# Performance work log

Measured on AMD Instinct MI355X. Metric: run time of the kernel, lower is better.

The kernel has to match this reference:

```python
import jax, jax.numpy as jnp
import numpy as np

NUM_USERS = 100000
NUM_ITEMS = 50000
EMB = 64
N_EDGES = 4800000
N_NODES = NUM_USERS + NUM_ITEMS
NEG_SLOPE = 0.01  # torch F.leaky_relu default


def setup_inputs() -> dict:
    key = jax.random.key(0)
    ks = jax.random.split(key, 12)
    inp = {
        "user_indices": jnp.arange(NUM_USERS, dtype=jnp.int32),
        "item_indices": jnp.arange(NUM_ITEMS, dtype=jnp.int32),
        "adj_rows": jax.random.randint(ks[0], (N_EDGES,), 0, N_NODES, dtype=jnp.int32),
        "adj_cols": jax.random.randint(ks[1], (N_EDGES,), 0, N_NODES, dtype=jnp.int32),
        "adj_vals": jax.random.uniform(ks[2], (N_EDGES,), dtype=jnp.float32),
        "user_emb": jax.random.normal(ks[3], (NUM_USERS, EMB), dtype=jnp.float32),
        "item_emb": jax.random.normal(ks[4], (NUM_ITEMS, EMB), dtype=jnp.float32),
    }
    # two propagation layers (layers=[64,64,64] -> zip gives 2 Linear pairs)
    s = 1.0 / np.sqrt(EMB)
    for li, kb in zip(range(2), range(5, 12, 4)):
        inp[f"W_gc{li}"] = jax.random.uniform(ks[kb], (EMB, EMB), jnp.float32, -s, s)
        inp[f"b_gc{li}"] = jax.random.uniform(ks[kb + 1], (EMB,), jnp.float32, -s, s)
        inp[f"W_bi{li}"] = jax.random.uniform(ks[kb + 2], (EMB, EMB), jnp.float32, -s, s)
        inp[f"b_bi{li}"] = jax.random.uniform(ks[kb + 3], (EMB,), jnp.float32, -s, s)
    return inp


def reference(user_indices, item_indices, adj_rows, adj_cols, adj_vals,
              user_emb, item_emb,
              W_gc0, b_gc0, W_bi0, b_bi0,
              W_gc1, b_gc1, W_bi1, b_bi1):
    ego = jnp.concatenate([user_emb[user_indices], item_emb[item_indices]], axis=0)  # [N, 64]
    n_nodes = ego.shape[0]
    all_embeddings = [ego]
    layer_params = [(W_gc0, b_gc0, W_bi0, b_bi0), (W_gc1, b_gc1, W_bi1, b_bi1)]
    for Wg, bg, Wb, bb in layer_params:
        # sparse adj @ ego : gather by col, scale by val, scatter-add by row
        side = jax.ops.segment_sum(adj_vals[:, None] * ego[adj_cols], adj_rows,
                                   num_segments=n_nodes)  # [N, 64]
        sum_emb = jax.nn.leaky_relu(side @ Wg.T + bg, NEG_SLOPE)
        bi_emb = jax.nn.leaky_relu((ego * side) @ Wb.T + bb, NEG_SLOPE)
        ego = sum_emb + bi_emb
        all_embeddings.append(ego)
    all_embeddings = jnp.concatenate(all_embeddings, axis=1)  # [N, 192]
    n_users = user_indices.shape[0]
    return all_embeddings[:n_users], all_embeddings[n_users:]
```

## Files before the change

### kernel.cpp

```cpp
#include <hip/hip_runtime.h>

#define NUSERS 100000
#define NITEMS 50000
#define NNODES 150000
#define EMB 64
#define NEDGES 4800000
#define OUTC 192
#define NEG_SLOPE 0.01f

#define BKT_SHIFT 10
#define NB 147
#define G 1024
#define EPB 4688
#define NSCAN (NB * G)
#define NSLICE 10
#define SLICE_SHIFT 14
#define NBINS (1024 * NSLICE)

typedef __attribute__((ext_vector_type(8))) short bf16x8;
typedef __attribute__((ext_vector_type(4))) float f32x4;

__device__ __forceinline__ unsigned short f2bf(float f) {
    unsigned u = __float_as_uint(f);
    unsigned r = (u + 0x7fffu + ((u >> 16) & 1u)) >> 16;
    return (unsigned short)r;
}
__device__ __forceinline__ float bf2f(short s) {
    return __uint_as_float(((unsigned)(unsigned short)s) << 16);
}

__global__ void build_ego(const int* __restrict__ ui, const int* __restrict__ ii,
                          const float* __restrict__ uemb, const float* __restrict__ iemb,
                          float* __restrict__ out, unsigned short* __restrict__ egoc) {
    int gid = blockIdx.x * blockDim.x + threadIdx.x;
    int r = gid >> 4, p = gid & 15;
    if (r >= NNODES) return;
    const float* src = (r < NUSERS) ? (uemb + (size_t)ui[r] * EMB)
                                    : (iemb + (size_t)ii[r - NUSERS] * EMB);
    float4 v = ((const float4*)src)[p];
    *(float4*)(out + (size_t)r * OUTC + p * 4) = v;
    ushort4 o;
    o.x = f2bf(v.x); o.y = f2bf(v.y); o.z = f2bf(v.z); o.w = f2bf(v.w);
    *(ushort4*)(egoc + (size_t)r * EMB + p * 4) = o;
}

__global__ void conv_w4(const float* __restrict__ s0, const float* __restrict__ s1,
                        const float* __restrict__ s2, const float* __restrict__ s3,
                        unsigned short* __restrict__ d0, unsigned short* __restrict__ d1,
                        unsigned short* __restrict__ d2, unsigned short* __restrict__ d3) {
    int i = blockIdx.x * 256 + threadIdx.x;
    if (i < 4096) {
        d0[i] = f2bf(s0[i]); d1[i] = f2bf(s1[i]);
        d2[i] = f2bf(s2[i]); d3[i] = f2bf(s3[i]);
    }
}

__global__ __launch_bounds__(256) void bucket_hist(const int* __restrict__ rows,
                                                   int* __restrict__ hist) {
    __shared__ int h[NB];
    int tid = threadIdx.x, blk = blockIdx.x;
    if (tid < NB) h[tid] = 0;
    __syncthreads();
    int q0 = blk * (EPB / 4), q1 = q0 + (EPB / 4);
    const int qmax = NEDGES / 4;
    if (q1 > qmax) q1 = qmax;
    for (int q = q0 + tid; q < q1; q += 256) {
        int4 r4 = ((const int4*)rows)[q];
        atomicAdd(&h[r4.x >> BKT_SHIFT], 1);
        atomicAdd(&h[r4.y >> BKT_SHIFT], 1);
        atomicAdd(&h[r4.z >> BKT_SHIFT], 1);
        atomicAdd(&h[r4.w >> BKT_SHIFT], 1);
    }
    __syncthreads();
    if (tid < NB) hist[(size_t)tid * G + blk] = h[tid];
}

__global__ void scan_chunk(const int* __restrict__ counts, int* __restrict__ outp,
                           int* __restrict__ blksum, int n) {
    __shared__ int buf[1024];
    int tid = threadIdx.x;
    int gid = blockIdx.x * 1024 + tid;
    int v = (gid < n) ? counts[gid] : 0;
    buf[tid] = v;
    __syncthreads();
    for (int off = 1; off < 1024; off <<= 1) {
        int t = (tid >= off) ? buf[tid - off] : 0;
        __syncthreads();
        buf[tid] += t;
        __syncthreads();
    }
    if (gid < n) outp[gid + 1] = buf[tid];
    if (tid == 1023) blksum[blockIdx.x] = buf[tid];
}

__global__ void scan_sums(int* __restrict__ blksum, int n) {
    __shared__ int buf[256];
    int tid = threadIdx.x;
    int v = (tid < n) ? blksum[tid] : 0;
    buf[tid] = v;
    __syncthreads();
    for (int off = 1; off < 256; off <<= 1) {
        int t = (tid >= off) ? buf[tid - off] : 0;
        __syncthreads();
        buf[tid] += t;
        __syncthreads();
    }
    if (tid < n) blksum[tid] = buf[tid] - v;
}

__global__ void add_offsets(int* __restrict__ outp, const int* __restrict__ blksum, int n) {
    int gid = blockIdx.x * 1024 + threadIdx.x;
    if (gid < n) outp[gid + 1] += blksum[blockIdx.x];
    if (gid == 0) outp[0] = 0;
}

__global__ __launch_bounds__(256) void bucket_scatter(
        const int* __restrict__ rows, const int* __restrict__ cols,
        const float* __restrict__ vals, const int* __restrict__ base,
        int2* __restrict__ bedge) {
    __shared__ int cur[NB];
    int tid = threadIdx.x, blk = blockIdx.x;
    if (tid < NB) cur[tid] = base[(size_t)tid * G + blk];
    __syncthreads();
    int q0 = blk * (EPB / 4), q1 = q0 + (EPB / 4);
    const int qmax = NEDGES / 4;
    if (q1 > qmax) q1 = qmax;
    for (int q = q0 + tid; q < q1; q += 256) {
        int4   r4 = ((const int4*)rows)[q];
        int4   c4 = ((const int4*)cols)[q];
        float4 v4 = ((const float4*)vals)[q];
        int s0 = atomicAdd(&cur[r4.x >> BKT_SHIFT], 1);
        bedge[s0] = make_int2(c4.x | ((r4.x & 1023) << 18), __float_as_int(v4.x));
        int s1 = atomicAdd(&cur[r4.y >> BKT_SHIFT], 1);
        bedge[s1] = make_int2(c4.y | ((r4.y & 1023) << 18), __float_as_int(v4.y));
        int s2 = atomicAdd(&cur[r4.z >> BKT_SHIFT], 1);
        bedge[s2] = make_int2(c4.z | ((r4.z & 1023) << 18), __float_as_int(v4.z));
        int s3 = atomicAdd(&cur[r4.w >> BKT_SHIFT], 1);
        bedge[s3] = make_int2(c4.w | ((r4.w & 1023) << 18), __float_as_int(v4.w));
    }
}

__global__ __launch_bounds__(1024) void bucket_csr(
        const int2* __restrict__ bedge, const int* __restrict__ base,
        int* __restrict__ rowptr, int2* __restrict__ csr) {
    __shared__ int h[NBINS];
    __shared__ int tsum[1024];
    int tid = threadIdx.x, bkt = blockIdx.x;
    int s  = base[(size_t)bkt * G];
    int e2 = base[(size_t)(bkt + 1) * G];
    for (int i = tid; i < NBINS; i += 1024) h[i] = 0;
    __syncthreads();
    for (int i = s + tid; i < e2; i += 1024) {
        int x = bedge[i].x;
        int bin = (x >> 18) * NSLICE + (((unsigned)x & 0x3FFFFu) >> SLICE_SHIFT);
        atomicAdd(&h[bin], 1);
    }
    __syncthreads();
    int b0 = tid * NSLICE;
    int cnt[NSLICE];
    int run = 0;
    #pragma unroll
    for (int i = 0; i < NSLICE; ++i) { cnt[i] = h[b0 + i]; run += cnt[i]; }
    tsum[tid] = run;
    __syncthreads();
    for (int off = 1; off < 1024; off <<= 1) {
        int t = (tid >= off) ? tsum[tid - off] : 0;
        __syncthreads();
        tsum[tid] += t;
        __syncthreads();
    }
    int excl = s + tsum[tid] - run;
    int rbase = bkt << BKT_SHIFT;
    if (rbase + tid < NNODES) rowptr[rbase + tid] = excl;
    if (bkt == NB - 1 && tid == 0) rowptr[NNODES] = NEDGES;
    #pragma unroll
    for (int i = 0; i < NSLICE; ++i) { int c = cnt[i]; h[b0 + i] = excl; excl += c; }
    __syncthreads();
    for (int i = s + tid; i < e2; i += 1024) {
        int2 t = bedge[i];
        int bin = (t.x >> 18) * NSLICE + (((unsigned)t.x & 0x3FFFFu) >> SLICE_SHIFT);
        int slot = atomicAdd(&h[bin], 1);
        csr[slot] = make_int2(t.x & 0x3FFFF, t.y);
    }
}

#define ACC8(g, v)                                              \
    a0 = fmaf(v, __uint_as_float((g).x << 16), a0);             \
    a1 = fmaf(v, __uint_as_float((g).x & 0xffff0000u), a1);     \
    a2 = fmaf(v, __uint_as_float((g).y << 16), a2);             \
    a3 = fmaf(v, __uint_as_float((g).y & 0xffff0000u), a3);     \
    a4 = fmaf(v, __uint_as_float((g).z << 16), a4);             \
    a5 = fmaf(v, __uint_as_float((g).z & 0xffff0000u), a5);     \
    a6 = fmaf(v, __uint_as_float((g).w << 16), a6);             \
    a7 = fmaf(v, __uint_as_float((g).w & 0xffff0000u), a7);

__global__ __launch_bounds__(512) void spmm_gather(
        const int* __restrict__ rowptr, const int2* __restrict__ csr,
        const unsigned short* __restrict__ egoc,
        unsigned short* __restrict__ sideb,
        int strideE) {
    int tid = blockIdx.x * blockDim.x + threadIdx.x;
    int row = tid >> 3;
    int dg  = tid & 7;
    if (row >= NNODES) return;
    int s = rowptr[row], e = rowptr[row + 1];
    const uint4* egc = (const uint4*)egoc;
    float a0 = 0.f, a1 = 0.f, a2 = 0.f, a3 = 0.f,
          a4 = 0.f, a5 = 0.f, a6 = 0.f, a7 = 0.f;
    for (int b = s; b < e; b += 4) {
        int i1 = b + 1 < e ? b + 1 : e - 1;
        int i2 = b + 2 < e ? b + 2 : e - 1;
        int i3 = b + 3 < e ? b + 3 : e - 1;
        int2 cv0 = csr[b], cv1 = csr[i1], cv2 = csr[i2], cv3 = csr[i3];
        float v0 = __int_as_float(cv0.y);
        float v1 = (b + 1 < e) ? __int_as_float(cv1.y) : 0.f;
        float v2 = (b + 2 < e) ? __int_as_float(cv2.y) : 0.f;
        float v3 = (b + 3 < e) ? __int_as_float(cv3.y) : 0.f;
        uint4 g0 = egc[(size_t)cv0.x * 8 + dg];
        uint4 g1 = egc[(size_t)cv1.x * 8 + dg];
        uint4 g2 = egc[(size_t)cv2.x * 8 + dg];
        uint4 g3 = egc[(size_t)cv3.x * 8 + dg];
        ACC8(g0, v0); ACC8(g1, v1); ACC8(g2, v2); ACC8(g3, v3);
    }
    uint p0 = (unsigned)f2bf(a0) | ((unsigned)f2bf(a1) << 16);
    uint p1 = (unsigned)f2bf(a2) | ((unsigned)f2bf(a3) << 16);
    uint p2 = (unsigned)f2bf(a4) | ((unsigned)f2bf(a5) << 16);
    uint p3 = (unsigned)f2bf(a6) | ((unsigned)f2bf(a7) << 16);
    uint4 st = make_uint4(p0, p1, p2, p3);
    *(uint4*)(sideb + (size_t)row * strideE + dg * 8) = st;
}

__global__ __launch_bounds__(256) void dense_mfma(
        const unsigned short* __restrict__ sideb, int sStrideE,
        const unsigned short* __restrict__ egoc,
        const unsigned short* __restrict__ wg,
        const unsigned short* __restrict__ wb,
        const float* __restrict__ bg, const float* __restrict__ bb,
        float* __restrict__ outCol,
        unsigned short* __restrict__ egocNew) {
    int lane = threadIdx.x & 63;
    int ct   = (threadIdx.x >> 6) * 16;
    int rtile = blockIdx.x * 16;
    int ar = lane & 15, kg = lane >> 4;
    bf16x8 sfrag[2], pfrag[2], wgf[2], wbf[2];
    #pragma unroll
    for (int t = 0; t < 2; ++t) {
        int koff = kg * 8 + 32 * t;
        bf16x8 sv = *(const bf16x8*)(sideb + (size_t)(rtile + ar) * sStrideE + koff);
        bf16x8 ev = *(const bf16x8*)(egoc  + (size_t)(rtile + ar) * EMB + koff);
        sfrag[t] = sv;
        bf16x8 pv;
        #pragma unroll
        for (int j = 0; j < 8; ++j)
            pv[j] = (short)f2bf(bf2f(sv[j]) * bf2f(ev[j]));
        pfrag[t] = pv;
        wgf[t] = *(const bf16x8*)(wg + (size_t)(ct + ar) * EMB + koff);
        wbf[t] = *(const bf16x8*)(wb + (size_t)(ct + ar) * EMB + koff);
    }
    f32x4 accg = {0.f, 0.f, 0.f, 0.f}, accb = {0.f, 0.f, 0.f, 0.f};
    accg = __builtin_amdgcn_mfma_f32_16x16x32_bf16(sfrag[0], wgf[0], accg, 0, 0, 0);
    accg = __builtin_amdgcn_mfma_f32_16x16x32_bf16(sfrag[1], wgf[1], accg, 0, 0, 0);
    accb = __builtin_amdgcn_mfma_f32_16x16x32_bf16(pfrag[0], wbf[0], accb, 0, 0, 0);
    accb = __builtin_amdgcn_mfma_f32_16x16x32_bf16(pfrag[1], wbf[1], accb, 0, 0, 0);
    int c = ct + ar;
    float biasg = bg[c], biasb = bb[c];
    #pragma unroll
    for (int i = 0; i < 4; ++i) {
        int r = rtile + kg * 4 + i;
        float g = accg[i] + biasg; g = (g > 0.f) ? g : NEG_SLOPE * g;
        float q = accb[i] + biasb; q = (q > 0.f) ? q : NEG_SLOPE * q;
        float nv = g + q;
        outCol[(size_t)r * OUTC + c] = nv;
        if (egocNew) egocNew[(size_t)r * EMB + c] = f2bf(nv);
    }
}

extern "C" void kernel_launch(void* const* d_in, const int* in_sizes, int n_in,
                              void* d_out, int out_size, void* d_ws, size_t ws_size,
                              hipStream_t stream) {
    const int*   ui   = (const int*)  d_in[0];
    const int*   ii   = (const int*)  d_in[1];
    const int*   rows = (const int*)  d_in[2];
    const int*   cols = (const int*)  d_in[3];
    const float* vals = (const float*)d_in[4];
    const float* uemb = (const float*)d_in[5];
    const float* iemb = (const float*)d_in[6];
    const float* Wg0 = (const float*)d_in[7],  *bg0 = (const float*)d_in[8];
    const float* Wb0 = (const float*)d_in[9],  *bb0 = (const float*)d_in[10];
    const float* Wg1 = (const float*)d_in[11], *bg1 = (const float*)d_in[12];
    const float* Wb1 = (const float*)d_in[13], *bb1 = (const float*)d_in[14];
    float* out = (float*)d_out;

    char* ws = (char*)d_ws;
    int2*  csr    = (int2*)ws; ws += (size_t)NEDGES * 8;
    char*  buf0   = ws;        ws += (size_t)NNODES * EMB * 2;
    char*  buf1   = ws;        ws += (size_t)NNODES * EMB * 2;
    unsigned short* egoc0 = (unsigned short*)ws; ws += (size_t)NNODES * EMB * 2;
    int*   rowptr = (int*) ws; ws += (size_t)(NNODES + 1) * 4;
    int*   hist   = (int*) ws; ws += (size_t)NSCAN * 4;
    int*   scanb  = (int*) ws; ws += (size_t)(NSCAN + 1) * 4;
    int*   blksum = (int*) ws; ws += 256 * 4;
    unsigned short* wgb0 = (unsigned short*)ws; ws += 4096 * 2;
    unsigned short* wbb0 = (unsigned short*)ws; ws += 4096 * 2;
    unsigned short* wgb1 = (unsigned short*)ws; ws += 4096 * 2;
    unsigned short* wbb1 = (unsigned short*)ws; ws += 4096 * 2;
    int2* bedge = (int2*)buf0;
    unsigned short* egoc1 = (unsigned short*)buf1;

    build_ego<<<(NNODES * 16 + 255) / 256, 256, 0, stream>>>(ui, ii, uemb, iemb,
                                                             out, egoc0);
    conv_w4<<<16, 256, 0, stream>>>(Wg0, Wb0, Wg1, Wb1, wgb0, wbb0, wgb1, wbb1);

    bucket_hist<<<G, 256, 0, stream>>>(rows, hist);
    scan_chunk<<<NSCAN / 1024, 1024, 0, stream>>>(hist, scanb, blksum, NSCAN);
    scan_sums<<<1, 256, 0, stream>>>(blksum, NSCAN / 1024);
    add_offsets<<<NSCAN / 1024, 1024, 0, stream>>>(scanb, blksum, NSCAN);
    bucket_scatter<<<G, 256, 0, stream>>>(rows, cols, vals, scanb, bedge);
    bucket_csr<<<NB, 1024, 0, stream>>>(bedge, scanb, rowptr, csr);

    unsigned short* side0 = (unsigned short*)((char*)out + 512);
    const int SIDE0_STRIDE = 384;
    spmm_gather<<<(NNODES * 8 + 511) / 512, 512, 0, stream>>>(rowptr, csr, egoc0,
                                                              side0, SIDE0_STRIDE);
    dense_mfma<<<NNODES / 16, 256, 0, stream>>>(side0, SIDE0_STRIDE, egoc0,
                                                wgb0, wbb0, bg0, bb0,
                                                out + 64, egoc1);

    unsigned short* side1 = (unsigned short*)buf0;
    spmm_gather<<<(NNODES * 8 + 511) / 512, 512, 0, stream>>>(rowptr, csr, egoc1,
                                                              side1, EMB);
    dense_mfma<<<NNODES / 16, 256, 0, stream>>>(side1, EMB, egoc1,
                                                wgb1, wbb1, bg1, bb1,
                                                out + 128, (unsigned short*)nullptr);
}
```

Baseline: 407.5 us.

## Sort rows by degree before SpMM gather to balance wavefront work

Adds a counting sort of rows by degree (histogram, scan, scatter) to build a row order, and the SpMM gather kernel now processes rows in that order. With 8 rows per wavefront, grouping rows of similar degree is meant to cut divergence where lanes wait on the longest row. The cost is three extra small kernels plus a memset, an indirect rowptr lookup, and scattered output writes and rowptr reads, which loses locality.

```diff
diff --git a/kernel.cpp b/kernel.cpp
--- a/kernel.cpp
+++ b/kernel.cpp
@@ -16,6 +16,7 @@
 #define NSLICE 10
 #define SLICE_SHIFT 14
 #define NBINS (1024 * NSLICE)
+#define NDEG 128
 
 typedef __attribute__((ext_vector_type(8))) short bf16x8;
 typedef __attribute__((ext_vector_type(4))) float f32x4;
@@ -184,6 +185,62 @@
     }
 }
 
+__global__ __launch_bounds__(1024) void deg_hist(const int* __restrict__ rowptr,
+                                                 int* __restrict__ ghist) {
+    __shared__ int h[NDEG];
+    int tid = threadIdx.x;
+    int r = blockIdx.x * 1024 + tid;
+    if (tid < NDEG) h[tid] = 0;
+    __syncthreads();
+    if (r < NNODES) {
+        int d = rowptr[r + 1] - rowptr[r];
+        if (d > NDEG - 1) d = NDEG - 1;
+        atomicAdd(&h[d], 1);
+    }
+    __syncthreads();
+    if (tid < NDEG && h[tid]) atomicAdd(&ghist[tid], h[tid]);
+}
+
+__global__ void deg_scan(int* __restrict__ ghist) {
+    __shared__ int buf[NDEG];
+    int tid = threadIdx.x;
+    int v = ghist[tid];
+    buf[tid] = v;
+    __syncthreads();
+    for (int off = 1; off < NDEG; off <<= 1) {
+        int t = (tid >= off) ? buf[tid - off] : 0;
+        __syncthreads();
+        buf[tid] += t;
+        __syncthreads();
+    }
+    ghist[tid] = buf[tid] - v;
+}
+
+__global__ __launch_bounds__(1024) void deg_scatter(const int* __restrict__ rowptr,
+                                                    int* __restrict__ gcur,
+                                                    int* __restrict__ rorder) {
+    __shared__ int h[NDEG];
+    __shared__ int basev[NDEG];
+    __shared__ int c2[NDEG];
+    int tid = threadIdx.x;
+    int r = blockIdx.x * 1024 + tid;
+    if (tid < NDEG) { h[tid] = 0; c2[tid] = 0; }
+    __syncthreads();
+    int d = -1;
+    if (r < NNODES) {
+        d = rowptr[r + 1] - rowptr[r];
+        if (d > NDEG - 1) d = NDEG - 1;
+        atomicAdd(&h[d], 1);
+    }
+    __syncthreads();
+    if (tid < NDEG && h[tid]) basev[tid] = atomicAdd(&gcur[tid], h[tid]);
+    __syncthreads();
+    if (r < NNODES) {
+        int rank = atomicAdd(&c2[d], 1);
+        rorder[basev[d] + rank] = r;
+    }
+}
+
 #define ACC8(g, v)                                              \
     a0 = fmaf(v, __uint_as_float((g).x << 16), a0);             \
     a1 = fmaf(v, __uint_as_float((g).x & 0xffff0000u), a1);     \
@@ -195,14 +252,16 @@
     a7 = fmaf(v, __uint_as_float((g).w & 0xffff0000u), a7);
 
 __global__ __launch_bounds__(512) void spmm_gather(
-        const int* __restrict__ rowptr, const int2* __restrict__ csr,
+        const int* __restrict__ rowptr, const int* __restrict__ rorder,
+        const int2* __restrict__ csr,
         const unsigned short* __restrict__ egoc,
         unsigned short* __restrict__ sideb,
         int strideE) {
     int tid = blockIdx.x * blockDim.x + threadIdx.x;
-    int row = tid >> 3;
+    int rid = tid >> 3;
     int dg  = tid & 7;
-    if (row >= NNODES) return;
+    if (rid >= NNODES) return;
+    int row = rorder[rid];
     int s = rowptr[row], e = rowptr[row + 1];
     const uint4* egc = (const uint4*)egoc;
     float a0 = 0.f, a1 = 0.f, a2 = 0.f, a3 = 0.f,
@@ -300,6 +359,8 @@
     int*   hist   = (int*) ws; ws += (size_t)NSCAN * 4;
     int*   scanb  = (int*) ws; ws += (size_t)(NSCAN + 1) * 4;
     int*   blksum = (int*) ws; ws += 256 * 4;
+    int*   rorder = (int*) ws; ws += (size_t)NNODES * 4;
+    int*   ghist  = (int*) ws; ws += NDEG * 4;
     unsigned short* wgb0 = (unsigned short*)ws; ws += 4096 * 2;
     unsigned short* wbb0 = (unsigned short*)ws; ws += 4096 * 2;
     unsigned short* wgb1 = (unsigned short*)ws; ws += 4096 * 2;
@@ -307,6 +368,8 @@
     int2* bedge = (int2*)buf0;
     unsigned short* egoc1 = (unsigned short*)buf1;
 
+    const int RBLK = (NNODES + 1023) / 1024;
+
     build_ego<<<(NNODES * 16 + 255) / 256, 256, 0, stream>>>(ui, ii, uemb, iemb,
                                                              out, egoc0);
     conv_w4<<<16, 256, 0, stream>>>(Wg0, Wb0, Wg1, Wb1, wgb0, wbb0, wgb1, wbb1);
@@ -318,17 +381,22 @@
     bucket_scatter<<<G, 256, 0, stream>>>(rows, cols, vals, scanb, bedge);
     bucket_csr<<<NB, 1024, 0, stream>>>(bedge, scanb, rowptr, csr);
 
+    hipMemsetAsync(ghist, 0, NDEG * 4, stream);
+    deg_hist<<<RBLK, 1024, 0, stream>>>(rowptr, ghist);
+    deg_scan<<<1, NDEG, 0, stream>>>(ghist);
+    deg_scatter<<<RBLK, 1024, 0, stream>>>(rowptr, ghist, rorder);
+
     unsigned short* side0 = (unsigned short*)((char*)out + 512);
     const int SIDE0_STRIDE = 384;
-    spmm_gather<<<(NNODES * 8 + 511) / 512, 512, 0, stream>>>(rowptr, csr, egoc0,
-                                                              side0, SIDE0_STRIDE);
+    spmm_gather<<<(NNODES * 8 + 511) / 512, 512, 0, stream>>>(rowptr, rorder, csr,
+                                                              egoc0, side0, SIDE0_STRIDE);
     dense_mfma<<<NNODES / 16, 256, 0, stream>>>(side0, SIDE0_STRIDE, egoc0,
                                                 wgb0, wbb0, bg0, bb0,
                                                 out + 64, egoc1);
 
     unsigned short* side1 = (unsigned short*)buf0;
-    spmm_gather<<<(NNODES * 8 + 511) / 512, 512, 0, stream>>>(rowptr, csr, egoc1,
-                                                              side1, EMB);
+    spmm_gather<<<(NNODES * 8 + 511) / 512, 512, 0, stream>>>(rowptr, rorder, csr,
+                                                              egoc1, side1, EMB);
     dense_mfma<<<NNODES / 16, 256, 0, stream>>>(side1, EMB, egoc1,
                                                 wgb1, wbb1, bg1, bb1,
                                                 out + 128, (unsigned short*)nullptr);
```

Result: slower. 427.4 us (+4.9%).
